# Kernel tuning notes

Measured on AMD Instinct MI355X. Metric: run time of the kernel, lower is better.

The kernel has to match this reference:

```python
import jax, jax.numpy as jnp
import numpy as np

M_POW = 4   # m: number of visual-graph powers
N_POW = 4   # n: number of text-graph powers
T = 32      # temporal length, forced by torch.eye(32) in GraphFusion
EPS_BN = 1e-5


def conv1d_same(x, w, b):
    # x: (B, Cin, L), w: (Cout, Cin, 3) -> (B, Cout, L), padding=1
    y = jax.lax.conv_general_dilated(x, w, window_strides=(1,), padding=[(1, 1)],
                                     dimension_numbers=("NCH", "OIH", "NCH"))
    return y + b[None, :, None]


def setup_inputs() -> dict:
    key = jax.random.key(0)
    ks = jax.random.split(key, 10)
    b, c = 128, 5
    d = {}
    d["v_feature"] = jax.random.normal(ks[0], (b, c, T, 2048), jnp.float32)
    d["t_feature"] = jax.random.normal(ks[1], (b, c, T, 768), jnp.float32)
    # Temporal embedding convs (Conv1d k=3, pad=1)
    d["wv"] = jax.random.normal(ks[2], (32, 2048, 3), jnp.float32) * 0.02
    d["bv"] = jnp.zeros((32,), jnp.float32)
    d["wt"] = jax.random.normal(ks[3], (32, 768, 3), jnp.float32) * 0.02
    d["bt"] = jnp.zeros((32,), jnp.float32)
    # GraphFusion learned (m, n) bilinear matrix: torch.normal(0, 1)
    d["fusion_a"] = jax.random.normal(ks[4], (M_POW, N_POW), jnp.float32)
    # NormalHead (BN-WVAD style, in_channel=32, hidden 2 -> 1 -> 1, all k=1 convs)
    d["w1"] = jax.random.normal(ks[5], (2, 32), jnp.float32) * 0.1
    d["b1"] = jnp.zeros((2,), jnp.float32)
    d["g1"] = jnp.ones((2,), jnp.float32)
    d["be1"] = jnp.zeros((2,), jnp.float32)
    d["w2"] = jax.random.normal(ks[6], (1, 2), jnp.float32) * 0.1
    d["b2"] = jnp.zeros((1,), jnp.float32)
    d["g2"] = jnp.ones((1,), jnp.float32)
    d["be2"] = jnp.zeros((1,), jnp.float32)
    d["w3"] = jax.random.normal(ks[7], (1, 1), jnp.float32) * 0.1
    d["b3"] = jnp.zeros((1,), jnp.float32)
    return d


def _forward(v_feature, t_feature, wv, bv, wt, bt, fusion_a,
             w1, b1, g1, be1, w2, b2, g2, be2, w3, b3):
    b, c, t, feat_v = v_feature.shape
    B = b * c
    fv = v_feature.reshape(B, t, feat_v)
    ft = t_feature.reshape(B, t, t_feature.shape[3])
    # Temporal: permute -> conv1d(k=3,pad=1) -> relu -> permute
    fv = jax.nn.relu(conv1d_same(fv.transpose(0, 2, 1), wv, bv)).transpose(0, 2, 1)  # (B,t,32)
    ft = jax.nn.relu(conv1d_same(ft.transpose(0, 2, 1), wt, bt)).transpose(0, 2, 1)  # (B,t,32)

    # GraphFusion
    def l2n(x):
        return x / jnp.maximum(jnp.linalg.norm(x, axis=2, keepdims=True), 1e-12)
    f_v = l2n(fv)
    f_t = l2n(ft)
    a_v = jax.nn.relu(jnp.einsum('bid,bjd->bij', f_v, f_v))  # (B,t,t)
    a_t = jax.nn.relu(jnp.einsum('bid,bjd->bij', f_t, f_t))  # (B,t,t)
    eye = jnp.broadcast_to(jnp.eye(t, dtype=a_v.dtype), (B, t, t))
    # power 0 replaced by identity, as in the torch code
    av_p = jnp.stack([eye] + [a_v ** i for i in range(1, M_POW)], axis=0)  # (m,B,t,t)
    at_p = jnp.stack([eye] + [a_t ** j for j in range(1, N_POW)], axis=0)  # (n,B,t,t)
    # einsum('bijk,kl,blij->bij') with the permutes undone == 'kbij,kl,lbij->bij'
    a_fused = jnp.einsum('kbij,kl,lbij->bij', av_p, fusion_a, at_p)
    a_fused = jax.nn.relu(a_fused)
    a_fused = a_fused / (jnp.max(a_fused) + 0.01)

    # NormalHead on x = a_fused.permute(0,2,1) : (B, C=t, L=t)
    x = a_fused.transpose(0, 2, 1)

    def bn(h, g, beta):  # training-mode BatchNorm1d over (N, L) per channel
        mu = h.mean(axis=(0, 2), keepdims=True)
        var = h.var(axis=(0, 2), keepdims=True)
        return (h - mu) * jax.lax.rsqrt(var + EPS_BN) * g[None, :, None] + beta[None, :, None]

    x1 = jnp.einsum('oc,bcl->bol', w1, x) + b1[None, :, None]
    h1 = jax.nn.relu(bn(x1, g1, be1))
    x2 = jnp.einsum('oc,bcl->bol', w2, h1) + b2[None, :, None]
    h2 = jax.nn.relu(bn(x2, g2, be2))
    scores = jax.nn.sigmoid(jnp.einsum('oc,bcl->bol', w3, h2) + b3[None, :, None])  # (B,1,t)
    normal_scores = scores.reshape(b, c, t).mean(axis=1)  # (b, t), crop-averaged
    return (normal_scores, a_v, a_t, a_fused)


def reference(v_feature, t_feature, wv, bv, wt, bt, fusion_a,
              w1, b1, g1, be1, w2, b2, g2, be2, w3, b3):
    return _forward(v_feature, t_feature, wv, bv, wt, bt, fusion_a,
                    w1, b1, g1, be1, w2, b2, g2, be2, w3, b3)
```

## Files before the change

### kernel.cpp

```cpp
#include <hip/hip_runtime.h>
#include <hip/hip_bf16.h>
#include <math.h>


typedef __attribute__((ext_vector_type(8))) short short8;
typedef __attribute__((ext_vector_type(4))) float f32x4;

#define XROW 132

__device__ __forceinline__ unsigned short f2bf(float f) {
    __hip_bfloat16 h = __float2bfloat16(f);
    return *reinterpret_cast<unsigned short*>(&h);
}
__device__ __forceinline__ float bf2f(unsigned short u) {
    return __uint_as_float(((unsigned int)u) << 16);
}
__device__ __forceinline__ short8 lds_frag(const unsigned short* p) {
    union { uint2 u2[2]; short8 s; } r;
    r.u2[0] = *reinterpret_cast<const uint2*>(p);
    r.u2[1] = *reinterpret_cast<const uint2*>(p + 4);
    return r.s;
}
__device__ __forceinline__ short8 glb_frag(const unsigned short* p) {
    union { uint4 u; short8 s; } r;
    r.u = *reinterpret_cast<const uint4*>(p);
    return r.s;
}

__global__ __launch_bounds__(256) void pack_kernel(
    const float* __restrict__ wv, const float* __restrict__ wt,
    unsigned short* __restrict__ wvpk, unsigned short* __restrict__ wtpk,
    float* __restrict__ scal, float* __restrict__ fv, float* __restrict__ ft) {
    int gid = blockIdx.x * 256 + threadIdx.x;
    if (gid < 16) scal[gid] = 0.f;
    for (int i = gid; i < 655360; i += 270336) {
        fv[i] = 0.f;
        ft[i] = 0.f;
    }
    const int NV = 196608, NT = 73728;
    if (gid < NV) {
        int o = gid / 6144, rem = gid % 6144;
        int c = rem / 3, k = rem % 3;
        int s = c >> 5, cp = c & 31;
        float f = wv[gid];
        unsigned short h = f2bf(f);
        unsigned short l = f2bf(f - bf2f(h));
        int base = (s * 3 + k) * 2048 + o * 32 + cp;
        wvpk[base] = h;
        wvpk[base + 1024] = l;
    } else if (gid < NV + NT) {
        int g = gid - NV;
        int o = g / 2304, rem = g % 2304;
        int c = rem / 3, k = rem % 3;
        int s = c >> 5, cp = c & 31;
        float f = wt[g];
        unsigned short h = f2bf(f);
        unsigned short l = f2bf(f - bf2f(h));
        int base = (s * 3 + k) * 2048 + o * 32 + cp;
        wtpk[base] = h;
        wtpk[base + 1024] = l;
    }
}

__device__ __forceinline__ void conv_phase(
    const float* __restrict__ xb, int Cin,
    const unsigned short* __restrict__ wpk,
    unsigned short* hiT, unsigned short* loT,
    float* __restrict__ yout, int tid, int wave, int lane, int part) {
    __syncthreads();
    if (tid < XROW) {
        hiT[tid] = 0; hiT[33 * XROW + tid] = 0;
        loT[tid] = 0; loT[33 * XROW + tid] = 0;
    }
    f32x4 acc0 = {0.f, 0.f, 0.f, 0.f};
    f32x4 acc1 = {0.f, 0.f, 0.f, 0.f};
    int tm = wave & 1, tn = wave >> 1;
    int m = lane & 15, quad = lane >> 4;
    int c4 = tid & 31, tg = tid >> 5;
    int nchunk = Cin >> 7;
    int ch0 = (nchunk * part) >> 2;
    int ch1 = (nchunk * (part + 1)) >> 2;
    for (int ch = ch0; ch < ch1; ++ch) {
        int c0 = ch << 7;
        __syncthreads();
#pragma unroll
        for (int pass = 0; pass < 4; ++pass) {
            int t = tg + (pass << 3);
            const float4 xq = *reinterpret_cast<const float4*>(
                xb + (size_t)t * Cin + c0 + (c4 << 2));
            unsigned short h0 = f2bf(xq.x), h1 = f2bf(xq.y);
            unsigned short h2 = f2bf(xq.z), h3 = f2bf(xq.w);
            unsigned short l0 = f2bf(xq.x - bf2f(h0));
            unsigned short l1 = f2bf(xq.y - bf2f(h1));
            unsigned short l2 = f2bf(xq.z - bf2f(h2));
            unsigned short l3 = f2bf(xq.w - bf2f(h3));
            int widx = (t + 1) * XROW + (c4 << 2);
            *reinterpret_cast<uint2*>(hiT + widx) =
                make_uint2(h0 | ((unsigned int)h1 << 16), h2 | ((unsigned int)h3 << 16));
            *reinterpret_cast<uint2*>(loT + widx) =
                make_uint2(l0 | ((unsigned int)l1 << 16), l2 | ((unsigned int)l3 << 16));
        }
        __syncthreads();
        int sbase = c0 >> 5;
        int arow0 = (tm << 4) + m;
        int bofs = ((tn << 4) + m) * 32 + (quad << 3);
#pragma unroll
        for (int sl = 0; sl < 4; ++sl) {
            int acol = (sl << 5) + (quad << 3);
            const unsigned short* bbase = wpk + (size_t)(sbase + sl) * 6144 + bofs;
#pragma unroll
            for (int k = 0; k < 3; ++k) {
                short8 Ah = lds_frag(hiT + (arow0 + k) * XROW + acol);
                short8 Al = lds_frag(loT + (arow0 + k) * XROW + acol);
                short8 Bh = glb_frag(bbase + k * 2048);
                short8 Bl = glb_frag(bbase + k * 2048 + 1024);
                acc0 = __builtin_amdgcn_mfma_f32_16x16x32_bf16(Ah, Bh, acc0, 0, 0, 0);
                acc1 = __builtin_amdgcn_mfma_f32_16x16x32_bf16(Ah, Bl, acc1, 0, 0, 0);
                acc1 = __builtin_amdgcn_mfma_f32_16x16x32_bf16(Al, Bh, acc1, 0, 0, 0);
            }
        }
    }
    int ocol = (tn << 4) + m;
#pragma unroll
    for (int r = 0; r < 4; ++r) {
        int t = (tm << 4) + (quad << 2) + r;
        atomicAdd(&yout[t * 32 + ocol], acc0[r] + acc1[r]);
    }
}

__global__ __launch_bounds__(256, 4) void conv_mfma_kernel(
    const float* __restrict__ xv, const unsigned short* __restrict__ wvpk,
    const float* __restrict__ xt, const unsigned short* __restrict__ wtpk,
    float* __restrict__ yv, float* __restrict__ yt) {
    __shared__ unsigned short hiT[34 * XROW], loT[34 * XROW];
    int bx = blockIdx.x;
    int b = bx >> 2, part = bx & 3;
    int tid = threadIdx.x;
    int wave = tid >> 6, lane = tid & 63;
    conv_phase(xv + (size_t)b * 32 * 2048, 2048, wvpk, hiT, loT,
               yv + (size_t)b * 1024, tid, wave, lane, part);
    conv_phase(xt + (size_t)b * 32 * 768, 768, wtpk, hiT, loT,
               yt + (size_t)b * 1024, tid, wave, lane, part);
}

__global__ __launch_bounds__(256) void s2_kernel(
    const float* __restrict__ fvp, const float* __restrict__ ftp,
    const float* __restrict__ bv, const float* __restrict__ bt,
    const float* __restrict__ fuse, float* __restrict__ out_av,
    float* __restrict__ out_at, float* __restrict__ out_af,
    unsigned int* __restrict__ maxslot) {
    int b = blockIdx.x, tid = threadIdx.x;
    __shared__ float Fv[32][33], Ft[32][33], inv[64], wmax[4];
#pragma unroll
    for (int e = 0; e < 4; ++e) {
        int idx = tid + 256 * e;
        int i = idx >> 5, j = idx & 31;
        Fv[i][j] = fmaxf(fvp[b * 1024 + idx] + bv[j], 0.f);
        Ft[i][j] = fmaxf(ftp[b * 1024 + idx] + bt[j], 0.f);
    }
    __syncthreads();
    {
        int row = tid >> 3, cg = (tid & 7) * 4;
        float sv = 0.f, st = 0.f;
#pragma unroll
        for (int q = 0; q < 4; ++q) {
            float v = Fv[row][cg + q]; sv = fmaf(v, v, sv);
            float u = Ft[row][cg + q]; st = fmaf(u, u, st);
        }
        sv += __shfl_xor(sv, 1); sv += __shfl_xor(sv, 2); sv += __shfl_xor(sv, 4);
        st += __shfl_xor(st, 1); st += __shfl_xor(st, 2); st += __shfl_xor(st, 4);
        if ((tid & 7) == 0) {
            inv[row]      = rsqrtf(fmaxf(sv, 1e-24f));
            inv[32 + row] = rsqrtf(fmaxf(st, 1e-24f));
        }
    }
    __syncthreads();
    float fa[16];
#pragma unroll
    for (int q = 0; q < 16; ++q) fa[q] = fuse[q];
    float lmax = 0.f;
#pragma unroll
    for (int e = 0; e < 4; ++e) {
        int idx = tid + 256 * e;
        int i = idx >> 5, j = idx & 31;
        float dv = 0.f, dt_ = 0.f;
        for (int c = 0; c < 32; ++c) {
            dv  = fmaf(Fv[i][c], Fv[j][c], dv);
            dt_ = fmaf(Ft[i][c], Ft[j][c], dt_);
        }
        float av = fmaxf(dv  * inv[i] * inv[j], 0.f);
        float at = fmaxf(dt_ * inv[32 + i] * inv[32 + j], 0.f);
        out_av[b * 1024 + idx] = av;
        out_at[b * 1024 + idx] = at;
        float pv0 = (i == j) ? 1.f : 0.f;
        float pv1 = av, pv2 = av * av, pv3 = pv2 * av;
        float pt1 = at, pt2 = at * at, pt3 = pt2 * at;
        float af = 0.f;
        af += (fa[0] * pv0 + fa[4] * pv1 + fa[8]  * pv2 + fa[12] * pv3) * pv0;
        af += (fa[1] * pv0 + fa[5] * pv1 + fa[9]  * pv2 + fa[13] * pv3) * pt1;
        af += (fa[2] * pv0 + fa[6] * pv1 + fa[10] * pv2 + fa[14] * pv3) * pt2;
        af += (fa[3] * pv0 + fa[7] * pv1 + fa[11] * pv2 + fa[15] * pv3) * pt3;
        float r = fmaxf(af, 0.f);
        out_af[b * 1024 + idx] = r;
        lmax = fmaxf(lmax, r);
    }
    for (int off = 1; off < 64; off <<= 1)
        lmax = fmaxf(lmax, __shfl_xor(lmax, off));
    if ((tid & 63) == 0) wmax[tid >> 6] = lmax;
    __syncthreads();
    if (tid == 0) {
        float mx = fmaxf(fmaxf(wmax[0], wmax[1]), fmaxf(wmax[2], wmax[3]));
        atomicMax(maxslot, __float_as_uint(mx));
    }
}

__global__ __launch_bounds__(256) void s3_kernel(
    float* __restrict__ af, const float* __restrict__ w1,
    const float* __restrict__ b1, float* __restrict__ x1,
    float* __restrict__ scal) {
    int b = blockIdx.x, tid = threadIdx.x;
    __shared__ float A[32][33];
    float inv = 1.0f / (__uint_as_float(((const unsigned int*)scal)[0]) + 0.01f);
#pragma unroll
    for (int e = 0; e < 4; ++e) {
        int idx = tid + 256 * e;
        float v = af[b * 1024 + idx] * inv;
        af[b * 1024 + idx] = v;
        A[idx >> 5][idx & 31] = v;
    }
    __syncthreads();
    if (tid < 64) {
        int o = tid >> 5, l = tid & 31;
        float s = b1[o];
        for (int c = 0; c < 32; ++c) s = fmaf(w1[o * 32 + c], A[l][c], s);
        x1[(size_t)(b * 2 + o) * 32 + l] = s;
        float s1 = s, s2 = s * s;
        for (int off = 1; off < 32; off <<= 1) {
            s1 += __shfl_xor(s1, off);
            s2 += __shfl_xor(s2, off);
        }
        if (l == 0) {
            atomicAdd(&scal[1 + o], s1);
            atomicAdd(&scal[3 + o], s2);
        }
    }
}

__global__ __launch_bounds__(256) void s4_kernel(
    const float* __restrict__ x1, const float* __restrict__ g1,
    const float* __restrict__ be1, const float* __restrict__ w2,
    const float* __restrict__ b2, float* __restrict__ x2,
    float* __restrict__ scal) {
    int idx = blockIdx.x * 256 + threadIdx.x;
    const float N = 20480.f;
    float mu0 = scal[1] / N, mu1 = scal[2] / N;
    float va0 = scal[3] / N - mu0 * mu0, va1 = scal[4] / N - mu1 * mu1;
    float rs0 = rsqrtf(va0 + 1e-5f), rs1 = rsqrtf(va1 + 1e-5f);
    int b = idx >> 5, l = idx & 31;
    float h0 = fmaxf((x1[(size_t)(b * 2 + 0) * 32 + l] - mu0) * rs0 * g1[0] + be1[0], 0.f);
    float h1 = fmaxf((x1[(size_t)(b * 2 + 1) * 32 + l] - mu1) * rs1 * g1[1] + be1[1], 0.f);
    float v = w2[0] * h0 + w2[1] * h1 + b2[0];
    x2[idx] = v;
    float s1 = v, s2 = v * v;
    for (int off = 1; off < 64; off <<= 1) {
        s1 += __shfl_xor(s1, off);
        s2 += __shfl_xor(s2, off);
    }
    __shared__ float ps[4][2];
    int lane = threadIdx.x & 63, w = threadIdx.x >> 6;
    if (lane == 0) { ps[w][0] = s1; ps[w][1] = s2; }
    __syncthreads();
    if (threadIdx.x == 0) {
        atomicAdd(&scal[5], ps[0][0] + ps[1][0] + ps[2][0] + ps[3][0]);
        atomicAdd(&scal[6], ps[0][1] + ps[1][1] + ps[2][1] + ps[3][1]);
    }
}

__global__ __launch_bounds__(256) void s5_kernel(
    const float* __restrict__ x2, const float* __restrict__ g2,
    const float* __restrict__ be2, const float* __restrict__ w3,
    const float* __restrict__ b3, float* __restrict__ ns,
    const float* __restrict__ scal) {
    int idx = blockIdx.x * 256 + threadIdx.x;
    const float N = 20480.f;
    float mu = scal[5] / N;
    float var = scal[6] / N - mu * mu;
    float rs = rsqrtf(var + 1e-5f);
    int bb = idx >> 5, t = idx & 31;
    float s = 0.f;
#pragma unroll
    for (int crop = 0; crop < 5; ++crop) {
        int b = bb * 5 + crop;
        float h = fmaxf((x2[b * 32 + t] - mu) * rs * g2[0] + be2[0], 0.f);
        float z = w3[0] * h + b3[0];
        s += 1.f / (1.f + expf(-z));
    }
    ns[idx] = s * 0.2f;
}

extern "C" void kernel_launch(void* const* d_in, const int* in_sizes, int n_in,
                              void* d_out, int out_size, void* d_ws, size_t ws_size,
                              hipStream_t stream) {
    const float* v_feat = (const float*)d_in[0];
    const float* t_feat = (const float*)d_in[1];
    const float* wv  = (const float*)d_in[2];
    const float* bv  = (const float*)d_in[3];
    const float* wt  = (const float*)d_in[4];
    const float* bt  = (const float*)d_in[5];
    const float* fuse= (const float*)d_in[6];
    const float* w1  = (const float*)d_in[7];
    const float* b1  = (const float*)d_in[8];
    const float* g1  = (const float*)d_in[9];
    const float* be1 = (const float*)d_in[10];
    const float* w2  = (const float*)d_in[11];
    const float* b2  = (const float*)d_in[12];
    const float* g2  = (const float*)d_in[13];
    const float* be2 = (const float*)d_in[14];
    const float* w3  = (const float*)d_in[15];
    const float* b3  = (const float*)d_in[16];

    float* ws   = (float*)d_ws;
    float* scal = ws;
    unsigned short* wvpk = (unsigned short*)(ws + 16);
    unsigned short* wtpk = (unsigned short*)(ws + 16 + 196608);
    float* fv   = ws + 16 + 196608 + 73728;
    float* ft   = fv + 655360;
    float* x1   = ft + 655360;
    float* x2   = x1 + 40960;

    float* out_ns = (float*)d_out;
    float* out_av = out_ns + 4096;
    float* out_at = out_av + 655360;
    float* out_af = out_at + 655360;

    pack_kernel<<<1056, 256, 0, stream>>>(wv, wt, wvpk, wtpk, scal, fv, ft);
    conv_mfma_kernel<<<2560, 256, 0, stream>>>(v_feat, wvpk, t_feat, wtpk, fv, ft);
    s2_kernel<<<640, 256, 0, stream>>>(fv, ft, bv, bt, fuse, out_av, out_at,
                                       out_af, (unsigned int*)scal);
    s3_kernel<<<640, 256, 0, stream>>>(out_af, w1, b1, x1, scal);
    s4_kernel<<<80, 256, 0, stream>>>(x1, g1, be1, w2, b2, x2, scal);
    s5_kernel<<<16, 256, 0, stream>>>(x2, g2, be2, w3, b3, out_ns, scal);
}
```

Baseline: 389.0 us.

## Prefetch next conv input chunk into registers and coalesce packed weight layout

The conv phase now loads the next 128-channel chunk of input features into registers while the current chunk's MFMAs run, so global load latency overlaps compute. The packed bf16 hi/lo weights are reordered so each wave's B fragment is a contiguous 16-byte-per-lane block, making those global loads coalesced. LDS row padding goes from 132 to 136 so A fragments can be read with a single 128-bit LDS load. In exchange the kernel holds more registers for the prefetched float4s, which may press against the 4-blocks-per-CU launch bound.

```diff
diff --git a/kernel.cpp b/kernel.cpp
--- a/kernel.cpp
+++ b/kernel.cpp
@@ -6,7 +6,7 @@
 typedef __attribute__((ext_vector_type(8))) short short8;
 typedef __attribute__((ext_vector_type(4))) float f32x4;
 
-#define XROW 132
+#define XROW 136
 
 __device__ __forceinline__ unsigned short f2bf(float f) {
     __hip_bfloat16 h = __float2bfloat16(f);
@@ -16,9 +16,8 @@
     return __uint_as_float(((unsigned int)u) << 16);
 }
 __device__ __forceinline__ short8 lds_frag(const unsigned short* p) {
-    union { uint2 u2[2]; short8 s; } r;
-    r.u2[0] = *reinterpret_cast<const uint2*>(p);
-    r.u2[1] = *reinterpret_cast<const uint2*>(p + 4);
+    union { uint4 u; short8 s; } r;
+    r.u = *reinterpret_cast<const uint4*>(p);
     return r.s;
 }
 __device__ __forceinline__ short8 glb_frag(const unsigned short* p) {
@@ -42,23 +41,25 @@
         int o = gid / 6144, rem = gid % 6144;
         int c = rem / 3, k = rem % 3;
         int s = c >> 5, cp = c & 31;
+        int tn = o >> 4, m = o & 15, quad = cp >> 3, j = cp & 7;
         float f = wv[gid];
         unsigned short h = f2bf(f);
         unsigned short l = f2bf(f - bf2f(h));
-        int base = (s * 3 + k) * 2048 + o * 32 + cp;
+        int base = (s * 3 + k) * 2048 + tn * 1024 + ((quad << 4) + m) * 8 + j;
         wvpk[base] = h;
-        wvpk[base + 1024] = l;
+        wvpk[base + 512] = l;
     } else if (gid < NV + NT) {
         int g = gid - NV;
         int o = g / 2304, rem = g % 2304;
         int c = rem / 3, k = rem % 3;
         int s = c >> 5, cp = c & 31;
+        int tn = o >> 4, m = o & 15, quad = cp >> 3, j = cp & 7;
         float f = wt[g];
         unsigned short h = f2bf(f);
         unsigned short l = f2bf(f - bf2f(h));
-        int base = (s * 3 + k) * 2048 + o * 32 + cp;
+        int base = (s * 3 + k) * 2048 + tn * 1024 + ((quad << 4) + m) * 8 + j;
         wtpk[base] = h;
-        wtpk[base + 1024] = l;
+        wtpk[base + 512] = l;
     }
 }
 
@@ -67,43 +68,61 @@
     const unsigned short* __restrict__ wpk,
     unsigned short* hiT, unsigned short* loT,
     float* __restrict__ yout, int tid, int wave, int lane, int part) {
-    __syncthreads();
-    if (tid < XROW) {
-        hiT[tid] = 0; hiT[33 * XROW + tid] = 0;
-        loT[tid] = 0; loT[33 * XROW + tid] = 0;
-    }
-    f32x4 acc0 = {0.f, 0.f, 0.f, 0.f};
-    f32x4 acc1 = {0.f, 0.f, 0.f, 0.f};
     int tm = wave & 1, tn = wave >> 1;
     int m = lane & 15, quad = lane >> 4;
     int c4 = tid & 31, tg = tid >> 5;
     int nchunk = Cin >> 7;
     int ch0 = (nchunk * part) >> 2;
     int ch1 = (nchunk * (part + 1)) >> 2;
+
+    const float* xbase = xb + (c4 << 2);
+    float4 xq0, xq1, xq2, xq3;
+    {
+        const float* p = xbase + (size_t)(ch0 << 7);
+        xq0 = *reinterpret_cast<const float4*>(p + (size_t)tg * Cin);
+        xq1 = *reinterpret_cast<const float4*>(p + (size_t)(tg + 8) * Cin);
+        xq2 = *reinterpret_cast<const float4*>(p + (size_t)(tg + 16) * Cin);
+        xq3 = *reinterpret_cast<const float4*>(p + (size_t)(tg + 24) * Cin);
+    }
+    __syncthreads();
+    if (tid < XROW) {
+        hiT[tid] = 0; hiT[33 * XROW + tid] = 0;
+        loT[tid] = 0; loT[33 * XROW + tid] = 0;
+    }
+    f32x4 acc0 = {0.f, 0.f, 0.f, 0.f};
+    f32x4 acc1 = {0.f, 0.f, 0.f, 0.f};
+
+    auto stage = [&](const float4& xq, int t) {
+        unsigned short h0 = f2bf(xq.x), h1 = f2bf(xq.y);
+        unsigned short h2 = f2bf(xq.z), h3 = f2bf(xq.w);
+        unsigned short l0 = f2bf(xq.x - bf2f(h0));
+        unsigned short l1 = f2bf(xq.y - bf2f(h1));
+        unsigned short l2 = f2bf(xq.z - bf2f(h2));
+        unsigned short l3 = f2bf(xq.w - bf2f(h3));
+        int widx = (t + 1) * XROW + (c4 << 2);
+        *reinterpret_cast<uint2*>(hiT + widx) =
+            make_uint2(h0 | ((unsigned int)h1 << 16), h2 | ((unsigned int)h3 << 16));
+        *reinterpret_cast<uint2*>(loT + widx) =
+            make_uint2(l0 | ((unsigned int)l1 << 16), l2 | ((unsigned int)l3 << 16));
+    };
+
     for (int ch = ch0; ch < ch1; ++ch) {
-        int c0 = ch << 7;
         __syncthreads();
-#pragma unroll
-        for (int pass = 0; pass < 4; ++pass) {
-            int t = tg + (pass << 3);
-            const float4 xq = *reinterpret_cast<const float4*>(
-                xb + (size_t)t * Cin + c0 + (c4 << 2));
-            unsigned short h0 = f2bf(xq.x), h1 = f2bf(xq.y);
-            unsigned short h2 = f2bf(xq.z), h3 = f2bf(xq.w);
-            unsigned short l0 = f2bf(xq.x - bf2f(h0));
-            unsigned short l1 = f2bf(xq.y - bf2f(h1));
-            unsigned short l2 = f2bf(xq.z - bf2f(h2));
-            unsigned short l3 = f2bf(xq.w - bf2f(h3));
-            int widx = (t + 1) * XROW + (c4 << 2);
-            *reinterpret_cast<uint2*>(hiT + widx) =
-                make_uint2(h0 | ((unsigned int)h1 << 16), h2 | ((unsigned int)h3 << 16));
-            *reinterpret_cast<uint2*>(loT + widx) =
-                make_uint2(l0 | ((unsigned int)l1 << 16), l2 | ((unsigned int)l3 << 16));
-        }
+        stage(xq0, tg);
+        stage(xq1, tg + 8);
+        stage(xq2, tg + 16);
+        stage(xq3, tg + 24);
         __syncthreads();
-        int sbase = c0 >> 5;
+        if (ch + 1 < ch1) {
+            const float* p = xbase + (size_t)((ch + 1) << 7);
+            xq0 = *reinterpret_cast<const float4*>(p + (size_t)tg * Cin);
+            xq1 = *reinterpret_cast<const float4*>(p + (size_t)(tg + 8) * Cin);
+            xq2 = *reinterpret_cast<const float4*>(p + (size_t)(tg + 16) * Cin);
+            xq3 = *reinterpret_cast<const float4*>(p + (size_t)(tg + 24) * Cin);
+        }
+        int sbase = ch << 2;
         int arow0 = (tm << 4) + m;
-        int bofs = ((tn << 4) + m) * 32 + (quad << 3);
+        int bofs = (tn << 10) + (lane << 3);
 #pragma unroll
         for (int sl = 0; sl < 4; ++sl) {
             int acol = (sl << 5) + (quad << 3);
@@ -112,8 +131,8 @@
             for (int k = 0; k < 3; ++k) {
                 short8 Ah = lds_frag(hiT + (arow0 + k) * XROW + acol);
                 short8 Al = lds_frag(loT + (arow0 + k) * XROW + acol);
-                short8 Bh = glb_frag(bbase + k * 2048);
-                short8 Bl = glb_frag(bbase + k * 2048 + 1024);
+                short8 Bh = glb_frag(bbase + (k << 11));
+                short8 Bl = glb_frag(bbase + (k << 11) + 512);
                 acc0 = __builtin_amdgcn_mfma_f32_16x16x32_bf16(Ah, Bh, acc0, 0, 0, 0);
                 acc1 = __builtin_amdgcn_mfma_f32_16x16x32_bf16(Ah, Bl, acc1, 0, 0, 0);
                 acc1 = __builtin_amdgcn_mfma_f32_16x16x32_bf16(Al, Bh, acc1, 0, 0, 0);
```

New measurement: 380.9 us. 1.02x faster.

## Reuse weight fragments across four batch items and prefetch activations in conv kernel

Applied to the files above, without the earlier changes.

Each conv block now handles four batch items per channel chunk, loading the bf16 hi/lo weight fragments into registers once per chunk and reusing them across the four items. The packed weight layout is reordered so each lane reads a contiguous 16-byte fragment, and the next item's activations are prefetched into registers while the current one is staged. The grid shrinks from 2560 to 640 blocks and launch bounds drop to 2 waves per SIMD, because the held weight fragments and four accumulator sets raise register pressure. The risks are lower occupancy and an uneven split of the text-feature chunks across the four parts.

```diff
diff --git a/kernel.cpp b/kernel.cpp
--- a/kernel.cpp
+++ b/kernel.cpp
@@ -42,105 +42,140 @@
         int o = gid / 6144, rem = gid % 6144;
         int c = rem / 3, k = rem % 3;
         int s = c >> 5, cp = c & 31;
+        int tn = o >> 4, m = o & 15, quad = cp >> 3, j = cp & 7;
         float f = wv[gid];
         unsigned short h = f2bf(f);
         unsigned short l = f2bf(f - bf2f(h));
-        int base = (s * 3 + k) * 2048 + o * 32 + cp;
+        int base = (s * 3 + k) * 2048 + tn * 1024 + ((quad << 4) + m) * 8 + j;
         wvpk[base] = h;
-        wvpk[base + 1024] = l;
+        wvpk[base + 512] = l;
     } else if (gid < NV + NT) {
         int g = gid - NV;
         int o = g / 2304, rem = g % 2304;
         int c = rem / 3, k = rem % 3;
         int s = c >> 5, cp = c & 31;
+        int tn = o >> 4, m = o & 15, quad = cp >> 3, j = cp & 7;
         float f = wt[g];
         unsigned short h = f2bf(f);
         unsigned short l = f2bf(f - bf2f(h));
-        int base = (s * 3 + k) * 2048 + o * 32 + cp;
+        int base = (s * 3 + k) * 2048 + tn * 1024 + ((quad << 4) + m) * 8 + j;
         wtpk[base] = h;
-        wtpk[base + 1024] = l;
-    }
-}
-
-__device__ __forceinline__ void conv_phase(
-    const float* __restrict__ xb, int Cin,
+        wtpk[base + 512] = l;
+    }
+}
+
+__device__ __forceinline__ void stage_row(const float4& xq, int t, int c4,
+                                          unsigned short* hiT,
+                                          unsigned short* loT) {
+    unsigned short h0 = f2bf(xq.x), h1 = f2bf(xq.y);
+    unsigned short h2 = f2bf(xq.z), h3 = f2bf(xq.w);
+    unsigned short l0 = f2bf(xq.x - bf2f(h0));
+    unsigned short l1 = f2bf(xq.y - bf2f(h1));
+    unsigned short l2 = f2bf(xq.z - bf2f(h2));
+    unsigned short l3 = f2bf(xq.w - bf2f(h3));
+    int widx = (t + 1) * XROW + (c4 << 2);
+    *reinterpret_cast<uint2*>(hiT + widx) =
+        make_uint2(h0 | ((unsigned int)h1 << 16), h2 | ((unsigned int)h3 << 16));
+    *reinterpret_cast<uint2*>(loT + widx) =
+        make_uint2(l0 | ((unsigned int)l1 << 16), l2 | ((unsigned int)l3 << 16));
+}
+
+__device__ __forceinline__ void conv_item(
+    const float* __restrict__ xb0, int Cin, int ch0, int ch1,
     const unsigned short* __restrict__ wpk,
     unsigned short* hiT, unsigned short* loT,
-    float* __restrict__ yout, int tid, int wave, int lane, int part) {
+    float* __restrict__ yout0, int tid, int wave, int lane) {
+    int tm = wave & 1, tn = wave >> 1;
+    int m = lane & 15, quad = lane >> 4;
+    int c4 = tid & 31, tg = tid >> 5;
+
     __syncthreads();
     if (tid < XROW) {
         hiT[tid] = 0; hiT[33 * XROW + tid] = 0;
         loT[tid] = 0; loT[33 * XROW + tid] = 0;
     }
-    f32x4 acc0 = {0.f, 0.f, 0.f, 0.f};
-    f32x4 acc1 = {0.f, 0.f, 0.f, 0.f};
-    int tm = wave & 1, tn = wave >> 1;
-    int m = lane & 15, quad = lane >> 4;
-    int c4 = tid & 31, tg = tid >> 5;
-    int nchunk = Cin >> 7;
-    int ch0 = (nchunk * part) >> 2;
-    int ch1 = (nchunk * (part + 1)) >> 2;
+    f32x4 a0[4], a1[4];
+#pragma unroll
+    for (int g = 0; g < 4; ++g) {
+        a0[g] = (f32x4){0.f, 0.f, 0.f, 0.f};
+        a1[g] = (f32x4){0.f, 0.f, 0.f, 0.f};
+    }
+    float4 q0, q1, q2, q3;
+    {
+        const float* p = xb0 + (size_t)(ch0 << 7) + (c4 << 2);
+        q0 = *reinterpret_cast<const float4*>(p + (size_t)tg * Cin);
+        q1 = *reinterpret_cast<const float4*>(p + (size_t)(tg + 8) * Cin);
+        q2 = *reinterpret_cast<const float4*>(p + (size_t)(tg + 16) * Cin);
+        q3 = *reinterpret_cast<const float4*>(p + (size_t)(tg + 24) * Cin);
+    }
     for (int ch = ch0; ch < ch1; ++ch) {
-        int c0 = ch << 7;
-        __syncthreads();
-#pragma unroll
-        for (int pass = 0; pass < 4; ++pass) {
-            int t = tg + (pass << 3);
-            const float4 xq = *reinterpret_cast<const float4*>(
-                xb + (size_t)t * Cin + c0 + (c4 << 2));
-            unsigned short h0 = f2bf(xq.x), h1 = f2bf(xq.y);
-            unsigned short h2 = f2bf(xq.z), h3 = f2bf(xq.w);
-            unsigned short l0 = f2bf(xq.x - bf2f(h0));
-            unsigned short l1 = f2bf(xq.y - bf2f(h1));
-            unsigned short l2 = f2bf(xq.z - bf2f(h2));
-            unsigned short l3 = f2bf(xq.w - bf2f(h3));
-            int widx = (t + 1) * XROW + (c4 << 2);
-            *reinterpret_cast<uint2*>(hiT + widx) =
-                make_uint2(h0 | ((unsigned int)h1 << 16), h2 | ((unsigned int)h3 << 16));
-            *reinterpret_cast<uint2*>(loT + widx) =
-                make_uint2(l0 | ((unsigned int)l1 << 16), l2 | ((unsigned int)l3 << 16));
-        }
-        __syncthreads();
-        int sbase = c0 >> 5;
-        int arow0 = (tm << 4) + m;
-        int bofs = ((tn << 4) + m) * 32 + (quad << 3);
-#pragma unroll
-        for (int sl = 0; sl < 4; ++sl) {
-            int acol = (sl << 5) + (quad << 3);
-            const unsigned short* bbase = wpk + (size_t)(sbase + sl) * 6144 + bofs;
+        short8 Bh[4][3], Bl[4][3];
+        const unsigned short* wbase =
+            wpk + (size_t)(ch << 2) * 6144 + (tn << 10) + (lane << 3);
+#pragma unroll
+        for (int sl = 0; sl < 4; ++sl)
 #pragma unroll
             for (int k = 0; k < 3; ++k) {
-                short8 Ah = lds_frag(hiT + (arow0 + k) * XROW + acol);
-                short8 Al = lds_frag(loT + (arow0 + k) * XROW + acol);
-                short8 Bh = glb_frag(bbase + k * 2048);
-                short8 Bl = glb_frag(bbase + k * 2048 + 1024);
-                acc0 = __builtin_amdgcn_mfma_f32_16x16x32_bf16(Ah, Bh, acc0, 0, 0, 0);
-                acc1 = __builtin_amdgcn_mfma_f32_16x16x32_bf16(Ah, Bl, acc1, 0, 0, 0);
-                acc1 = __builtin_amdgcn_mfma_f32_16x16x32_bf16(Al, Bh, acc1, 0, 0, 0);
+                Bh[sl][k] = glb_frag(wbase + sl * 6144 + (k << 11));
+                Bl[sl][k] = glb_frag(wbase + sl * 6144 + (k << 11) + 512);
             }
+#pragma unroll
+        for (int g = 0; g < 4; ++g) {
+            __syncthreads();
+            stage_row(q0, tg, c4, hiT, loT);
+            stage_row(q1, tg + 8, c4, hiT, loT);
+            stage_row(q2, tg + 16, c4, hiT, loT);
+            stage_row(q3, tg + 24, c4, hiT, loT);
+            int nch = ch + ((g + 1) >> 2), ng = (g + 1) & 3;
+            if (nch < ch1) {
+                const float* p = xb0 + (size_t)ng * 32 * Cin
+                                 + (size_t)(nch << 7) + (c4 << 2);
+                q0 = *reinterpret_cast<const float4*>(p + (size_t)tg * Cin);
+                q1 = *reinterpret_cast<const float4*>(p + (size_t)(tg + 8) * Cin);
+                q2 = *reinterpret_cast<const float4*>(p + (size_t)(tg + 16) * Cin);
+                q3 = *reinterpret_cast<const float4*>(p + (size_t)(tg + 24) * Cin);
+            }
+            __syncthreads();
+            int arow0 = (tm << 4) + m;
+#pragma unroll
+            for (int sl = 0; sl < 4; ++sl) {
+                int acol = (sl << 5) + (quad << 3);
+#pragma unroll
+                for (int k = 0; k < 3; ++k) {
+                    short8 Ah = lds_frag(hiT + (arow0 + k) * XROW + acol);
+                    short8 Al = lds_frag(loT + (arow0 + k) * XROW + acol);
+                    a0[g] = __builtin_amdgcn_mfma_f32_16x16x32_bf16(Ah, Bh[sl][k], a0[g], 0, 0, 0);
+                    a1[g] = __builtin_amdgcn_mfma_f32_16x16x32_bf16(Ah, Bl[sl][k], a1[g], 0, 0, 0);
+                    a1[g] = __builtin_amdgcn_mfma_f32_16x16x32_bf16(Al, Bh[sl][k], a1[g], 0, 0, 0);
+                }
+            }
         }
     }
     int ocol = (tn << 4) + m;
 #pragma unroll
-    for (int r = 0; r < 4; ++r) {
-        int t = (tm << 4) + (quad << 2) + r;
-        atomicAdd(&yout[t * 32 + ocol], acc0[r] + acc1[r]);
-    }
-}
-
-__global__ __launch_bounds__(256, 4) void conv_mfma_kernel(
+    for (int g = 0; g < 4; ++g)
+#pragma unroll
+        for (int r = 0; r < 4; ++r) {
+            int t = (tm << 4) + (quad << 2) + r;
+            atomicAdd(&yout0[g * 1024 + t * 32 + ocol], a0[g][r] + a1[g][r]);
+        }
+}
+
+__global__ __launch_bounds__(256, 2) void conv_mfma_kernel(
     const float* __restrict__ xv, const unsigned short* __restrict__ wvpk,
     const float* __restrict__ xt, const unsigned short* __restrict__ wtpk,
     float* __restrict__ yv, float* __restrict__ yt) {
     __shared__ unsigned short hiT[34 * XROW], loT[34 * XROW];
     int bx = blockIdx.x;
-    int b = bx >> 2, part = bx & 3;
+    int part = bx & 3;
+    int b0 = (bx >> 2) << 2;
     int tid = threadIdx.x;
     int wave = tid >> 6, lane = tid & 63;
-    conv_phase(xv + (size_t)b * 32 * 2048, 2048, wvpk, hiT, loT,
-               yv + (size_t)b * 1024, tid, wave, lane, part);
-    conv_phase(xt + (size_t)b * 32 * 768, 768, wtpk, hiT, loT,
-               yt + (size_t)b * 1024, tid, wave, lane, part);
+    conv_item(xv + (size_t)b0 * 65536, 2048, part << 2, (part << 2) + 4,
+              wvpk, hiT, loT, yv + (size_t)b0 * 1024, tid, wave, lane);
+    int t0 = (6 * part) >> 2, t1 = (6 * (part + 1)) >> 2;
+    conv_item(xt + (size_t)b0 * 24576, 768, t0, t1,
+              wtpk, hiT, loT, yt + (size_t)b0 * 1024, tid, wave, lane);
 }
 
 __global__ __launch_bounds__(256) void s2_kernel(
@@ -334,7 +369,7 @@
     float* out_af = out_at + 655360;
 
     pack_kernel<<<1056, 256, 0, stream>>>(wv, wt, wvpk, wtpk, scal, fv, ft);
-    conv_mfma_kernel<<<2560, 256, 0, stream>>>(v_feat, wvpk, t_feat, wtpk, fv, ft);
+    conv_mfma_kernel<<<640, 256, 0, stream>>>(v_feat, wvpk, t_feat, wtpk, fv, ft);
     s2_kernel<<<640, 256, 0, stream>>>(fv, ft, bv, bt, fuse, out_av, out_at,
                                        out_af, (unsigned int*)scal);
     s3_kernel<<<640, 256, 0, stream>>>(out_af, w1, b1, x1, scal);
```

After: 372.9 us. -4.1%, faster.

## Drop LDS staging in conv; load activations directly per wave and reuse weights across four batches

Applied to the files above, without the earlier changes.

The conv kernel no longer stages activations through shared memory with block-wide barriers. Each wave now loads its A fragments straight from global memory, with clamped row offsets and masks to handle the padding. Weights are repacked into an MFMA-fragment-friendly layout and held in registers across four batch items. This reduces weight reloads and removes the syncs, at the cost of redundant global activation reads (each row is read three times for the k taps), higher register pressure, and fewer blocks.

```diff
diff --git a/kernel.cpp b/kernel.cpp
--- a/kernel.cpp
+++ b/kernel.cpp
@@ -6,20 +6,12 @@
 typedef __attribute__((ext_vector_type(8))) short short8;
 typedef __attribute__((ext_vector_type(4))) float f32x4;
 
-#define XROW 132
-
 __device__ __forceinline__ unsigned short f2bf(float f) {
     __hip_bfloat16 h = __float2bfloat16(f);
     return *reinterpret_cast<unsigned short*>(&h);
 }
 __device__ __forceinline__ float bf2f(unsigned short u) {
     return __uint_as_float(((unsigned int)u) << 16);
-}
-__device__ __forceinline__ short8 lds_frag(const unsigned short* p) {
-    union { uint2 u2[2]; short8 s; } r;
-    r.u2[0] = *reinterpret_cast<const uint2*>(p);
-    r.u2[1] = *reinterpret_cast<const uint2*>(p + 4);
-    return r.s;
 }
 __device__ __forceinline__ short8 glb_frag(const unsigned short* p) {
     union { uint4 u; short8 s; } r;
@@ -42,105 +34,126 @@
         int o = gid / 6144, rem = gid % 6144;
         int c = rem / 3, k = rem % 3;
         int s = c >> 5, cp = c & 31;
+        int tn = o >> 4, m = o & 15, quad = cp >> 3, j = cp & 7;
         float f = wv[gid];
         unsigned short h = f2bf(f);
         unsigned short l = f2bf(f - bf2f(h));
-        int base = (s * 3 + k) * 2048 + o * 32 + cp;
+        int base = (s * 3 + k) * 2048 + tn * 1024 + ((quad << 4) + m) * 8 + j;
         wvpk[base] = h;
-        wvpk[base + 1024] = l;
+        wvpk[base + 512] = l;
     } else if (gid < NV + NT) {
         int g = gid - NV;
         int o = g / 2304, rem = g % 2304;
         int c = rem / 3, k = rem % 3;
         int s = c >> 5, cp = c & 31;
+        int tn = o >> 4, m = o & 15, quad = cp >> 3, j = cp & 7;
         float f = wt[g];
         unsigned short h = f2bf(f);
         unsigned short l = f2bf(f - bf2f(h));
-        int base = (s * 3 + k) * 2048 + o * 32 + cp;
+        int base = (s * 3 + k) * 2048 + tn * 1024 + ((quad << 4) + m) * 8 + j;
         wtpk[base] = h;
-        wtpk[base + 1024] = l;
-    }
-}
-
-__device__ __forceinline__ void conv_phase(
-    const float* __restrict__ xb, int Cin,
-    const unsigned short* __restrict__ wpk,
-    unsigned short* hiT, unsigned short* loT,
-    float* __restrict__ yout, int tid, int wave, int lane, int part) {
-    __syncthreads();
-    if (tid < XROW) {
-        hiT[tid] = 0; hiT[33 * XROW + tid] = 0;
-        loT[tid] = 0; loT[33 * XROW + tid] = 0;
-    }
-    f32x4 acc0 = {0.f, 0.f, 0.f, 0.f};
-    f32x4 acc1 = {0.f, 0.f, 0.f, 0.f};
-    int tm = wave & 1, tn = wave >> 1;
-    int m = lane & 15, quad = lane >> 4;
-    int c4 = tid & 31, tg = tid >> 5;
-    int nchunk = Cin >> 7;
-    int ch0 = (nchunk * part) >> 2;
-    int ch1 = (nchunk * (part + 1)) >> 2;
-    for (int ch = ch0; ch < ch1; ++ch) {
-        int c0 = ch << 7;
-        __syncthreads();
-#pragma unroll
-        for (int pass = 0; pass < 4; ++pass) {
-            int t = tg + (pass << 3);
-            const float4 xq = *reinterpret_cast<const float4*>(
-                xb + (size_t)t * Cin + c0 + (c4 << 2));
-            unsigned short h0 = f2bf(xq.x), h1 = f2bf(xq.y);
-            unsigned short h2 = f2bf(xq.z), h3 = f2bf(xq.w);
-            unsigned short l0 = f2bf(xq.x - bf2f(h0));
-            unsigned short l1 = f2bf(xq.y - bf2f(h1));
-            unsigned short l2 = f2bf(xq.z - bf2f(h2));
-            unsigned short l3 = f2bf(xq.w - bf2f(h3));
-            int widx = (t + 1) * XROW + (c4 << 2);
-            *reinterpret_cast<uint2*>(hiT + widx) =
-                make_uint2(h0 | ((unsigned int)h1 << 16), h2 | ((unsigned int)h3 << 16));
-            *reinterpret_cast<uint2*>(loT + widx) =
-                make_uint2(l0 | ((unsigned int)l1 << 16), l2 | ((unsigned int)l3 << 16));
-        }
-        __syncthreads();
-        int sbase = c0 >> 5;
-        int arow0 = (tm << 4) + m;
-        int bofs = ((tn << 4) + m) * 32 + (quad << 3);
-#pragma unroll
-        for (int sl = 0; sl < 4; ++sl) {
-            int acol = (sl << 5) + (quad << 3);
-            const unsigned short* bbase = wpk + (size_t)(sbase + sl) * 6144 + bofs;
+        wtpk[base + 512] = l;
+    }
+}
+
+__device__ __forceinline__ void conv_part(
+    const float* __restrict__ xb0, int Cin, int s0, int s1,
+    const unsigned short* __restrict__ wpk, float* __restrict__ yout,
+    int tm, int lane, int m, int quad,
+    const int* roff, const float* msk) {
+    f32x4 acc[4][2];
+#pragma unroll
+    for (int g = 0; g < 4; ++g)
+#pragma unroll
+        for (int tn = 0; tn < 2; ++tn)
+            acc[g][tn] = (f32x4){0.f, 0.f, 0.f, 0.f};
+
+    for (int s = s0; s < s1; ++s) {
+        int c0 = s << 5;
+        short8 Bh[2][3], Bl[2][3];
+        const unsigned short* wb = wpk + (size_t)s * 6144 + (lane << 3);
+#pragma unroll
+        for (int k = 0; k < 3; ++k)
+#pragma unroll
+            for (int tn = 0; tn < 2; ++tn) {
+                Bh[tn][k] = glb_frag(wb + (k << 11) + (tn << 10));
+                Bl[tn][k] = glb_frag(wb + (k << 11) + (tn << 10) + 512);
+            }
+#pragma unroll
+        for (int g = 0; g < 4; ++g) {
+            const float* xg = xb0 + (size_t)g * 32 * Cin + c0 + (quad << 3);
+            float4 xa[3][2];
 #pragma unroll
             for (int k = 0; k < 3; ++k) {
-                short8 Ah = lds_frag(hiT + (arow0 + k) * XROW + acol);
-                short8 Al = lds_frag(loT + (arow0 + k) * XROW + acol);
-                short8 Bh = glb_frag(bbase + k * 2048);
-                short8 Bl = glb_frag(bbase + k * 2048 + 1024);
-                acc0 = __builtin_amdgcn_mfma_f32_16x16x32_bf16(Ah, Bh, acc0, 0, 0, 0);
-                acc1 = __builtin_amdgcn_mfma_f32_16x16x32_bf16(Ah, Bl, acc1, 0, 0, 0);
-                acc1 = __builtin_amdgcn_mfma_f32_16x16x32_bf16(Al, Bh, acc1, 0, 0, 0);
+                const float* p = xg + (size_t)roff[k] * Cin;
+                xa[k][0] = *reinterpret_cast<const float4*>(p);
+                xa[k][1] = *reinterpret_cast<const float4*>(p + 4);
             }
-        }
-    }
-    int ocol = (tn << 4) + m;
-#pragma unroll
-    for (int r = 0; r < 4; ++r) {
-        int t = (tm << 4) + (quad << 2) + r;
-        atomicAdd(&yout[t * 32 + ocol], acc0[r] + acc1[r]);
-    }
-}
-
-__global__ __launch_bounds__(256, 4) void conv_mfma_kernel(
+#pragma unroll
+            for (int k = 0; k < 3; ++k) {
+                float f0 = xa[k][0].x * msk[k], f1 = xa[k][0].y * msk[k];
+                float f2 = xa[k][0].z * msk[k], f3 = xa[k][0].w * msk[k];
+                float f4 = xa[k][1].x * msk[k], f5 = xa[k][1].y * msk[k];
+                float f6 = xa[k][1].z * msk[k], f7 = xa[k][1].w * msk[k];
+                union { unsigned short u[8]; short8 s; } Ah, Al;
+                unsigned short h;
+                h = f2bf(f0); Ah.u[0] = h; Al.u[0] = f2bf(f0 - bf2f(h));
+                h = f2bf(f1); Ah.u[1] = h; Al.u[1] = f2bf(f1 - bf2f(h));
+                h = f2bf(f2); Ah.u[2] = h; Al.u[2] = f2bf(f2 - bf2f(h));
+                h = f2bf(f3); Ah.u[3] = h; Al.u[3] = f2bf(f3 - bf2f(h));
+                h = f2bf(f4); Ah.u[4] = h; Al.u[4] = f2bf(f4 - bf2f(h));
+                h = f2bf(f5); Ah.u[5] = h; Al.u[5] = f2bf(f5 - bf2f(h));
+                h = f2bf(f6); Ah.u[6] = h; Al.u[6] = f2bf(f6 - bf2f(h));
+                h = f2bf(f7); Ah.u[7] = h; Al.u[7] = f2bf(f7 - bf2f(h));
+#pragma unroll
+                for (int tn = 0; tn < 2; ++tn) {
+                    acc[g][tn] = __builtin_amdgcn_mfma_f32_16x16x32_bf16(
+                        Ah.s, Bh[tn][k], acc[g][tn], 0, 0, 0);
+                    acc[g][tn] = __builtin_amdgcn_mfma_f32_16x16x32_bf16(
+                        Ah.s, Bl[tn][k], acc[g][tn], 0, 0, 0);
+                    acc[g][tn] = __builtin_amdgcn_mfma_f32_16x16x32_bf16(
+                        Al.s, Bh[tn][k], acc[g][tn], 0, 0, 0);
+                }
+            }
+        }
+    }
+#pragma unroll
+    for (int g = 0; g < 4; ++g)
+#pragma unroll
+        for (int tn = 0; tn < 2; ++tn)
+#pragma unroll
+            for (int r = 0; r < 4; ++r) {
+                int trow = (tm << 4) + (quad << 2) + r;
+                atomicAdd(&yout[g * 1024 + trow * 32 + (tn << 4) + m],
+                          acc[g][tn][r]);
+            }
+}
+
+__global__ __launch_bounds__(256, 2) void conv_mfma_kernel(
     const float* __restrict__ xv, const unsigned short* __restrict__ wvpk,
     const float* __restrict__ xt, const unsigned short* __restrict__ wtpk,
     float* __restrict__ yv, float* __restrict__ yt) {
-    __shared__ unsigned short hiT[34 * XROW], loT[34 * XROW];
-    int bx = blockIdx.x;
-    int b = bx >> 2, part = bx & 3;
     int tid = threadIdx.x;
-    int wave = tid >> 6, lane = tid & 63;
-    conv_phase(xv + (size_t)b * 32 * 2048, 2048, wvpk, hiT, loT,
-               yv + (size_t)b * 1024, tid, wave, lane, part);
-    conv_phase(xt + (size_t)b * 32 * 768, 768, wtpk, hiT, loT,
-               yt + (size_t)b * 1024, tid, wave, lane, part);
+    int w = tid >> 6, lane = tid & 63;
+    int t = blockIdx.x * 4 + w;
+    int group = t >> 4, rem = t & 15;
+    int tm = rem >> 3, kpart = rem & 7;
+    int b0 = group << 2;
+    int m = lane & 15, quad = lane >> 4;
+
+    int roff[3];
+    float msk[3];
+#pragma unroll
+    for (int k = 0; k < 3; ++k) {
+        int r = (tm << 4) + m + k - 1;
+        msk[k] = (r >= 0 && r < 32) ? 1.f : 0.f;
+        roff[k] = r < 0 ? 0 : (r > 31 ? 31 : r);
+    }
+
+    conv_part(xv + (size_t)b0 * 65536, 2048, kpart << 3, (kpart << 3) + 8,
+              wvpk, yv + (size_t)b0 * 1024, tm, lane, m, quad, roff, msk);
+    conv_part(xt + (size_t)b0 * 24576, 768, kpart * 3, kpart * 3 + 3,
+              wtpk, yt + (size_t)b0 * 1024, tm, lane, m, quad, roff, msk);
 }
 
 __global__ __launch_bounds__(256) void s2_kernel(
@@ -334,7 +347,7 @@
     float* out_af = out_at + 655360;
 
     pack_kernel<<<1056, 256, 0, stream>>>(wv, wt, wvpk, wtpk, scal, fv, ft);
-    conv_mfma_kernel<<<2560, 256, 0, stream>>>(v_feat, wvpk, t_feat, wtpk, fv, ft);
+    conv_mfma_kernel<<<640, 256, 0, stream>>>(v_feat, wvpk, t_feat, wtpk, fv, ft);
     s2_kernel<<<640, 256, 0, stream>>>(fv, ft, bv, bt, fuse, out_av, out_at,
                                        out_af, (unsigned int*)scal);
     s3_kernel<<<640, 256, 0, stream>>>(out_af, w1, b1, x1, scal);
```

Measured after the change: 428.5 us. +10.1%, slower.
